# Performance work log

Measured on AMD Instinct MI355X. Metric: run time of the kernel, lower is better.

Reference implementation:

```python
import jax, jax.numpy as jnp
import numpy as np

# graph constants
B, V, CG, K, H, IN = 4, 6250, 25000, 3, 64, 2
NUM_LIT = B * 2 * V          # 50_000 literal nodes
NUM_CLS = B * CG             # 100_000 clause nodes
E = K * NUM_CLS              # 300_000 (l2c, c2l) edge pairs
NUM_ROUND = 3
DEMON = float(np.sqrt(H))    # self.demon = sqrt(hidden_size)


def setup_inputs() -> dict:
    key = jax.random.key(0)
    ks = jax.random.split(key, 12)
    rng = np.random.default_rng(0)
    # each clause has K literal endpoints; edges stay inside their own graph
    cls_idx = np.repeat(np.arange(NUM_CLS), K)
    g = cls_idx // CG
    lit_idx = g * 2 * V + rng.integers(0, 2 * V, size=E)

    def lin(k, fi, fo):
        return (jax.random.normal(k, (fi, fo), jnp.float32) / np.sqrt(fi)).astype(jnp.float32)

    return {
        "feat_l2c": jax.random.normal(ks[0], (E, IN), jnp.float32),
        "feat_c2l": jax.random.normal(ks[1], (E, IN), jnp.float32),
        "lit_idx": jnp.asarray(lit_idx, jnp.int32),
        "cls_idx": jnp.asarray(cls_idx, jnp.int32),
        "W_l2c_init": lin(ks[2], IN, H), "b_l2c_init": jnp.zeros((H,), jnp.float32),
        "W_c2l_init": lin(ks[3], IN, H), "b_c2l_init": jnp.zeros((H,), jnp.float32),
        "msgl_W": (jax.random.normal(ks[4], (3, H, H), jnp.float32) / np.sqrt(H)).astype(jnp.float32),
        "msgl_b": jnp.zeros((3, H), jnp.float32),
        "merge_W0": lin(ks[5], 2 * H, H), "merge_b0": jnp.zeros((H,), jnp.float32),
        "merge_Wr": (jax.random.normal(ks[6], (2, H, H), jnp.float32) / np.sqrt(H)).astype(jnp.float32),
        "merge_br": jnp.zeros((2, H), jnp.float32),
        "msgc_W": (jax.random.normal(ks[7], (3, H, H), jnp.float32) / np.sqrt(H)).astype(jnp.float32),
        "msgc_b": jnp.zeros((3, H), jnp.float32),
        "ro_W": (jax.random.normal(ks[8], (2, H, H), jnp.float32) / np.sqrt(H)).astype(jnp.float32),
        "ro_b": jnp.zeros((2, H), jnp.float32),
        "ro_W2": lin(ks[9], H, 1), "ro_b2": jnp.zeros((1,), jnp.float32),
    }


def _mlp3(x, W, b):  # 3-layer MLP, ReLU between layers (num_fc = 3)
    x = jax.nn.relu(x @ W[0] + b[0])
    x = jax.nn.relu(x @ W[1] + b[1])
    return x @ W[2] + b[2]


def reference(feat_l2c, feat_c2l, lit_idx, cls_idx,
              W_l2c_init, b_l2c_init, W_c2l_init, b_c2l_init,
              msgl_W, msgl_b, merge_W0, merge_b0, merge_Wr, merge_br,
              msgc_W, msgc_b, ro_W, ro_b, ro_W2, ro_b2):
    # init edge embeddings (l2c_init / c2l_init linear layers)
    h_l2c = feat_l2c @ W_l2c_init + b_l2c_init   # [E, H]
    h_c2l = feat_c2l @ W_c2l_init + b_c2l_init   # [E, H]

    for _ in range(NUM_ROUND):
        # literal update: aggregate incoming c2l messages, exclude self edge (BP-style)
        agg_l = jax.ops.segment_sum(h_c2l, lit_idx, num_segments=NUM_LIT)   # [NUM_LIT, H]
        m = _mlp3((agg_l[lit_idx] - h_c2l) / DEMON, msgl_W, msgl_b)          # [E, H]
        x = jax.nn.relu(jnp.concatenate([m, h_l2c], axis=-1) @ merge_W0 + merge_b0)
        x = jax.nn.relu(x @ merge_Wr[0] + merge_br[0])
        h_l2c = x @ merge_Wr[1] + merge_br[1]                                # l2c_merge_update
        # clause update
        agg_c = jax.ops.segment_sum(h_l2c, cls_idx, num_segments=NUM_CLS)   # [NUM_CLS, H]
        h_c2l = _mlp3((agg_c[cls_idx] - h_l2c) / DEMON, msgc_W, msgc_b)

    # u_add_e_sum with zero node feats == scatter-add edge emb to dst;
    # literal nodes only receive c2l edges
    l_emb = jax.ops.segment_sum(h_c2l, lit_idx, num_segments=NUM_LIT)        # [NUM_LIT, H]
    # segment_reduce(num_variable*2, ..., 'mean') over per-graph literal blocks (uniform sizes)
    l_mean = l_emb.reshape(B, 2 * V, H).mean(axis=1)                          # [B, H]
    x = jax.nn.relu(l_mean @ ro_W[0] + ro_b[0])
    x = jax.nn.relu(x @ ro_W[1] + ro_b[1])
    return jax.nn.sigmoid(x @ ro_W2 + ro_b2).squeeze(-1)                      # [B]
```

## Files before the change

### kernel.cpp

```cpp
#include <hip/hip_runtime.h>
#include <hip/hip_bf16.h>
#include <stdint.h>

#define EDGES   300000
#define NLIT    50000
#define NGRAPH  4
#define EPG     75000
#define HDIM    64

#define OFF_HL2C   0
#define OFF_HC2L   38400000
#define OFF_AGG    76800000
#define OFF_WT     89600000
#define OFF_ROACC  89681920
#define OFF_CNT    89682944
#define OFF_CSROFF 89882944
#define OFF_CURSOR 90082948
#define OFF_EIDX   90282948
#define OFF_BSUM   91482948
#define OFF_BBASE  91484000

#define WT_TOTAL    40960
#define WT_CLS_ELEM 28672

#define LIT_WBYTES (7 * 8192)
#define CLS_WBYTES (3 * 8192)
#define EPB3       512
#define GRID_EDGE  ((EDGES + EPB3 - 1) / EPB3)

#define SCAN_BLOCKS ((NLIT + 255) / 256)

typedef __attribute__((ext_vector_type(8)))  short          s16x8;
typedef __attribute__((ext_vector_type(8)))  unsigned short u16x8;
typedef __attribute__((ext_vector_type(4)))  unsigned short u16x4;
typedef __attribute__((ext_vector_type(4)))  float          f32x4;
typedef __attribute__((ext_vector_type(16))) float          f32x16;

__device__ __forceinline__ f32x16 mfma32(s16x8 a, s16x8 b, f32x16 c) {
    return __builtin_amdgcn_mfma_f32_32x32x16_bf16(a, b, c, 0, 0, 0);
}
__device__ __forceinline__ float bf2f(unsigned short s) {
    union { unsigned int u; float f; } v; v.u = ((unsigned int)s) << 16; return v.f;
}
__device__ __forceinline__ unsigned short f2bf(float f) {
    union { __hip_bfloat16 b; unsigned short s; } v;
    v.b = __float2bfloat16(f);
    return v.s;
}
__device__ __forceinline__ unsigned pk2(float a, float b) {
    return (unsigned)f2bf(a) | ((unsigned)f2bf(b) << 16);
}

__device__ __forceinline__ void layer32(const char* __restrict__ unitBase,
                                        const float* __restrict__ biasL,
                                        const s16x8 (&bin)[4], f32x16 (&acc)[2],
                                        int eL, int hi)
{
#pragma unroll
    for (int t = 0; t < 2; ++t)
#pragma unroll
        for (int g = 0; g < 4; ++g) {
            f32x4 bv = *(const f32x4*)(biasL + 32 * t + 8 * g + 4 * hi);
#pragma unroll
            for (int r = 0; r < 4; ++r) acc[t][4 * g + r] = bv[r];
        }
#pragma unroll
    for (int kb = 0; kb < 4; ++kb)
#pragma unroll
        for (int t = 0; t < 2; ++t) {
            int row = 32 * t + eL;
            s16x8 a = *(const s16x8*)(unitBase + row * 128 +
                                      ((32 * kb + 16 * hi) ^ ((row & 7) << 4)));
            acc[t] = mfma32(a, bin[kb], acc[t]);
        }
}

template<bool RELU>
__device__ __forceinline__ void relayout32(f32x16 (&acc)[2], s16x8 (&bout)[4],
                                           int bpidx, int hi)
{
    if (RELU) {
#pragma unroll
        for (int t = 0; t < 2; ++t)
#pragma unroll
            for (int i = 0; i < 16; ++i) acc[t][i] = fmaxf(acc[t][i], 0.f);
    }
#pragma unroll
    for (int kb = 0; kb < 4; ++kb) {
        int m0 = 2 * kb, m1 = 2 * kb + 1;
        int t0 = m0 >> 2, g0 = m0 & 3, t1 = m1 >> 2, g1 = m1 & 3;
        unsigned A0 = pk2(acc[t0][4 * g0 + 0], acc[t0][4 * g0 + 1]);
        unsigned A1 = pk2(acc[t0][4 * g0 + 2], acc[t0][4 * g0 + 3]);
        unsigned B0 = pk2(acc[t1][4 * g1 + 0], acc[t1][4 * g1 + 1]);
        unsigned B1 = pk2(acc[t1][4 * g1 + 2], acc[t1][4 * g1 + 3]);
        unsigned pA0 = (unsigned)__builtin_amdgcn_ds_bpermute(bpidx, (int)A0);
        unsigned pA1 = (unsigned)__builtin_amdgcn_ds_bpermute(bpidx, (int)A1);
        unsigned pB0 = (unsigned)__builtin_amdgcn_ds_bpermute(bpidx, (int)B0);
        unsigned pB1 = (unsigned)__builtin_amdgcn_ds_bpermute(bpidx, (int)B1);
        union { unsigned w[4]; s16x8 v; } u;
        u.w[0] = hi ? pB0 : A0;
        u.w[1] = hi ? pB1 : A1;
        u.w[2] = hi ? B0 : pA0;
        u.w[3] = hi ? B1 : pA1;
        bout[kb] = u.v;
    }
}

__device__ __forceinline__ void store32(const f32x16 (&acc)[2],
                                        unsigned short* __restrict__ dst, int hi)
{
#pragma unroll
    for (int t = 0; t < 2; ++t)
#pragma unroll
        for (int g = 0; g < 4; ++g) {
            u16x4 p;
#pragma unroll
            for (int r = 0; r < 4; ++r) p[r] = f2bf(acc[t][4 * g + r]);
            *(u16x4*)(dst + 32 * t + 8 * g + 4 * hi) = p;
        }
}

__global__ __launch_bounds__(256) void prep_weights(
    const float* __restrict__ msgl_W, const float* __restrict__ merge_W0,
    const float* __restrict__ merge_Wr, const float* __restrict__ msgc_W,
    unsigned short* __restrict__ wT)
{
    int gid = blockIdx.x * 256 + threadIdx.x;
    if (gid >= WT_TOTAL) return;
    int unit = gid >> 12;
    int o = (gid >> 6) & 63;
    int csw = gid & 63;
    int i = csw ^ ((o & 7) << 3);
    float v;
    if (unit < 3)       v = msgl_W[unit * 4096 + i * 64 + o];
    else if (unit < 5)  v = merge_W0[((unit - 3) * 64 + i) * 64 + o];
    else if (unit < 7)  v = merge_Wr[(unit - 5) * 4096 + i * 64 + o];
    else                v = msgc_W[(unit - 7) * 4096 + i * 64 + o];
    wT[gid] = f2bf(v);
}

__global__ __launch_bounds__(256) void csr_hist(const int* __restrict__ lit_idx,
                                                int* __restrict__ cnt)
{
    int e = blockIdx.x * 256 + threadIdx.x;
    if (e < EDGES) atomicAdd(&cnt[lit_idx[e]], 1);
}

__global__ __launch_bounds__(256) void scan1(const int* __restrict__ cnt,
                                             int* __restrict__ bsum)
{
    __shared__ int red[4];
    int i = blockIdx.x * 256 + threadIdx.x;
    int s = (i < NLIT) ? cnt[i] : 0;
#pragma unroll
    for (int off = 1; off < 64; off <<= 1) s += __shfl_xor(s, off, 64);
    if ((threadIdx.x & 63) == 0) red[threadIdx.x >> 6] = s;
    __syncthreads();
    if (threadIdx.x == 0) bsum[blockIdx.x] = red[0] + red[1] + red[2] + red[3];
}

__global__ __launch_bounds__(256) void scan2(const int* __restrict__ bsum,
                                             int* __restrict__ bbase)
{
    __shared__ int tmp[256];
    int t = threadIdx.x;
    int v = (t < SCAN_BLOCKS) ? bsum[t] : 0;
    tmp[t] = v;
    __syncthreads();
#pragma unroll
    for (int off = 1; off < 256; off <<= 1) {
        int add = (t >= off) ? tmp[t - off] : 0;
        __syncthreads();
        tmp[t] += add;
        __syncthreads();
    }
    if (t < SCAN_BLOCKS) bbase[t] = tmp[t] - v;
}

__global__ __launch_bounds__(256) void scan3(const int* __restrict__ cnt,
                                             const int* __restrict__ bbase,
                                             int* __restrict__ off,
                                             int* __restrict__ cursor)
{
    __shared__ int tmp[256];
    int t = threadIdx.x;
    int i = blockIdx.x * 256 + t;
    int v = (i < NLIT) ? cnt[i] : 0;
    tmp[t] = v;
    __syncthreads();
#pragma unroll
    for (int offs = 1; offs < 256; offs <<= 1) {
        int add = (t >= offs) ? tmp[t - offs] : 0;
        __syncthreads();
        tmp[t] += add;
        __syncthreads();
    }
    if (i < NLIT) {
        int ex = bbase[blockIdx.x] + tmp[t] - v;
        off[i] = ex; cursor[i] = ex;
    }
    if (i == NLIT - 1) off[NLIT] = EDGES;
}

__global__ __launch_bounds__(256) void csr_scatter(const int* __restrict__ lit_idx,
                                                   int* __restrict__ cursor,
                                                   int* __restrict__ eidx)
{
    int e = blockIdx.x * 256 + threadIdx.x;
    if (e >= EDGES) return;
    int pos = atomicAdd(&cursor[lit_idx[e]], 1);
    eidx[pos] = e;
}

__global__ __launch_bounds__(256) void aggregate(const unsigned short* __restrict__ h_c2l,
                                                 const int* __restrict__ off,
                                                 const int* __restrict__ eidx,
                                                 float* __restrict__ agg)
{
    int t = threadIdx.x;
    int lane8 = t & 7;
    int lit = blockIdx.x * 32 + (t >> 3);
    if (lit >= NLIT) return;
    int lo = off[lit], hi = off[lit + 1];
    float s[8] = {0, 0, 0, 0, 0, 0, 0, 0};
    int i = lo;
    for (; i + 4 <= hi; i += 4) {
        int e0 = eidx[i], e1 = eidx[i + 1], e2 = eidx[i + 2], e3 = eidx[i + 3];
        u16x8 v0 = *(const u16x8*)(h_c2l + e0 * 64 + lane8 * 8);
        u16x8 v1 = *(const u16x8*)(h_c2l + e1 * 64 + lane8 * 8);
        u16x8 v2 = *(const u16x8*)(h_c2l + e2 * 64 + lane8 * 8);
        u16x8 v3 = *(const u16x8*)(h_c2l + e3 * 64 + lane8 * 8);
#pragma unroll
        for (int j = 0; j < 8; ++j)
            s[j] += (bf2f(v0[j]) + bf2f(v1[j])) + (bf2f(v2[j]) + bf2f(v3[j]));
    }
    for (; i < hi; ++i) {
        int e = eidx[i];
        u16x8 hv = *(const u16x8*)(h_c2l + e * 64 + lane8 * 8);
#pragma unroll
        for (int j = 0; j < 8; ++j) s[j] += bf2f(hv[j]);
    }
    f32x4 a0, a1;
    a0[0] = s[0]; a0[1] = s[1]; a0[2] = s[2]; a0[3] = s[3];
    a1[0] = s[4]; a1[1] = s[5]; a1[2] = s[6]; a1[3] = s[7];
    *(f32x4*)(agg + lit * 64 + lane8 * 8)     = a0;
    *(f32x4*)(agg + lit * 64 + lane8 * 8 + 4) = a1;
}

__global__ __launch_bounds__(256) void init_kernel(
    const float* __restrict__ feat_l2c, const float* __restrict__ feat_c2l,
    const float* __restrict__ W_l2c, const float* __restrict__ b_l2c,
    const float* __restrict__ W_c2l, const float* __restrict__ b_c2l,
    unsigned short* __restrict__ h_l2c, unsigned short* __restrict__ h_c2l)
{
    int gid = blockIdx.x * 256 + threadIdx.x;
    if (gid >= EDGES * 8) return;
    int e = gid >> 3, fo = (gid & 7) << 3;
    float2 fl = *(const float2*)(feat_l2c + e * 2);
    float2 fc = *(const float2*)(feat_c2l + e * 2);

    u16x8 outl, outc;
#pragma unroll
    for (int j = 0; j < 8; ++j) {
        float wl0 = W_l2c[fo + j], wl1 = W_l2c[64 + fo + j];
        float wc0 = W_c2l[fo + j], wc1 = W_c2l[64 + fo + j];
        float vl = fl.x * wl0 + fl.y * wl1 + b_l2c[fo + j];
        float vc = fc.x * wc0 + fc.y * wc1 + b_c2l[fo + j];
        outl[j] = f2bf(vl);
        outc[j] = f2bf(vc);
    }
    *(u16x8*)(h_l2c + e * 64 + fo) = outl;
    *(u16x8*)(h_c2l + e * 64 + fo) = outc;
}

__global__ __launch_bounds__(1024, 4) void lit_update(
    const unsigned short* __restrict__ h_c2l,
    unsigned short* __restrict__ h_l2c,
    const float* __restrict__ agg,
    const int* __restrict__ lit_idx,
    const unsigned short* __restrict__ wT,
    const float* __restrict__ msgl_b,
    const float* __restrict__ merge_b0,
    const float* __restrict__ merge_br)
{
    __shared__ __align__(16) char lds[LIT_WBYTES + 384 * 4];
    int tid = threadIdx.x;
    for (int c = tid; c < LIT_WBYTES / 16; c += 1024)
        *(u16x8*)(lds + c * 16) = *(const u16x8*)(wT + c * 8);
    float* ldsBias = (float*)(lds + LIT_WBYTES);
    if (tid < 384) {
        float v;
        if (tid < 192)      v = msgl_b[tid];
        else if (tid < 256) v = merge_b0[tid - 192];
        else                v = merge_br[tid - 256];
        ldsBias[tid] = v;
    }
    __syncthreads();

    int wv = tid >> 6, lane = tid & 63;
    int eL = lane & 31, hi = lane >> 5;
    int bpidx = (lane ^ 32) << 2;
    int base = blockIdx.x * EPB3 + wv * 32;
    if (base >= EDGES) return;
    int e = base + eL;
    int lit = lit_idx[e];

    s16x8 hfrag[4];
#pragma unroll
    for (int k = 0; k < 4; ++k)
        hfrag[k] = *(const s16x8*)(h_l2c + e * 64 + 16 * k + 8 * hi);

    s16x8 binp[4];
#pragma unroll
    for (int k = 0; k < 4; ++k) {
        int f0 = 16 * k + 8 * hi;
        f32x4 a0 = *(const f32x4*)(agg + lit * 64 + f0);
        f32x4 a1 = *(const f32x4*)(agg + lit * 64 + f0 + 4);
        u16x8 hv = *(const u16x8*)(h_c2l + e * 64 + f0);
        s16x8 b;
#pragma unroll
        for (int j = 0; j < 4; ++j) b[j]     = (short)f2bf((a0[j] - bf2f(hv[j]))     * 0.125f);
#pragma unroll
        for (int j = 0; j < 4; ++j) b[4 + j] = (short)f2bf((a1[j] - bf2f(hv[4 + j])) * 0.125f);
        binp[k] = b;
    }

    f32x16 acc[2];
    s16x8 bf[4];
    layer32(lds,            ldsBias,       binp, acc, eL, hi);
    relayout32<true >(acc, bf, bpidx, hi);
    layer32(lds + 8192,     ldsBias + 64,  bf, acc, eL, hi);
    relayout32<true >(acc, bf, bpidx, hi);
    layer32(lds + 2 * 8192, ldsBias + 128, bf, acc, eL, hi);
    relayout32<false>(acc, bf, bpidx, hi);

#pragma unroll
    for (int t = 0; t < 2; ++t)
#pragma unroll
        for (int g = 0; g < 4; ++g) {
            f32x4 bv = *(const f32x4*)(ldsBias + 192 + 32 * t + 8 * g + 4 * hi);
#pragma unroll
            for (int r = 0; r < 4; ++r) acc[t][4 * g + r] = bv[r];
        }
#pragma unroll
    for (int kb = 0; kb < 8; ++kb) {
        const char* ub = lds + (3 + (kb >> 2)) * 8192;
        s16x8 bop = (kb < 4) ? bf[kb] : hfrag[kb - 4];
#pragma unroll
        for (int t = 0; t < 2; ++t) {
            int row = 32 * t + eL;
            s16x8 a = *(const s16x8*)(ub + row * 128 +
                                      ((32 * (kb & 3) + 16 * hi) ^ ((row & 7) << 4)));
            acc[t] = mfma32(a, bop, acc[t]);
        }
    }
    relayout32<true>(acc, bf, bpidx, hi);
    layer32(lds + 5 * 8192, ldsBias + 256, bf, acc, eL, hi);
    relayout32<true>(acc, bf, bpidx, hi);
    layer32(lds + 6 * 8192, ldsBias + 320, bf, acc, eL, hi);

    store32(acc, h_l2c + e * 64, hi);
}

__global__ __launch_bounds__(1024, 4) void clause_update(
    const unsigned short* __restrict__ h_l2c,
    unsigned short* __restrict__ h_c2l,
    const unsigned short* __restrict__ msgcT,
    const float* __restrict__ msgc_b)
{
    __shared__ __align__(16) char lds[CLS_WBYTES + 192 * 4];
    int tid = threadIdx.x;
    for (int c = tid; c < CLS_WBYTES / 16; c += 1024)
        *(u16x8*)(lds + c * 16) = *(const u16x8*)(msgcT + c * 8);
    float* ldsBias = (float*)(lds + CLS_WBYTES);
    if (tid < 192) ldsBias[tid] = msgc_b[tid];
    __syncthreads();

    int wv = tid >> 6, lane = tid & 63;
    int eL = lane & 31, hi = lane >> 5;
    int bpidx = (lane ^ 32) << 2;
    int base = blockIdx.x * EPB3 + wv * 32;
    if (base >= EDGES) return;
    int e = base + eL;

    int c3 = (e / 3) * 3;
    int d = e - c3;
    int e1 = c3 + (d == 0 ? 1 : 0);
    int e2 = c3 + (d == 2 ? 1 : 2);

    s16x8 binp[4];
#pragma unroll
    for (int k = 0; k < 4; ++k) {
        int f0 = 16 * k + 8 * hi;
        u16x8 h1 = *(const u16x8*)(h_l2c + e1 * 64 + f0);
        u16x8 h2 = *(const u16x8*)(h_l2c + e2 * 64 + f0);
        s16x8 b;
#pragma unroll
        for (int j = 0; j < 8; ++j)
            b[j] = (short)f2bf((bf2f(h1[j]) + bf2f(h2[j])) * 0.125f);
        binp[k] = b;
    }

    f32x16 acc[2];
    s16x8 bf[4];
    layer32(lds,            ldsBias,       binp, acc, eL, hi);
    relayout32<true>(acc, bf, bpidx, hi);
    layer32(lds + 8192,     ldsBias + 64,  bf, acc, eL, hi);
    relayout32<true>(acc, bf, bpidx, hi);
    layer32(lds + 2 * 8192, ldsBias + 128, bf, acc, eL, hi);

    store32(acc, h_c2l + e * 64, hi);
}

__global__ __launch_bounds__(256) void readout_sum(
    const unsigned short* __restrict__ h_c2l, float* __restrict__ ro_acc)
{
    __shared__ float lsum[32][64];
    int g = blockIdx.x >> 6, chunk = blockIdx.x & 63;
    int t = threadIdx.x;
    int fg = t & 7, el = t >> 3;
    float s[8] = {0, 0, 0, 0, 0, 0, 0, 0};
    for (int idx = chunk * 32 + el; idx < EPG; idx += 2048) {
        u16x8 hv = *(const u16x8*)(h_c2l + (g * EPG + idx) * 64 + fg * 8);
#pragma unroll
        for (int j = 0; j < 8; ++j) s[j] += bf2f(hv[j]);
    }
#pragma unroll
    for (int j = 0; j < 8; ++j) lsum[el][fg * 8 + j] = s[j];
    __syncthreads();
    if (t < 64) {
        float tot = 0.f;
#pragma unroll 8
        for (int r = 0; r < 32; ++r) tot += lsum[r][t];
        atomicAdd(&ro_acc[g * 64 + t], tot);
    }
}

__global__ __launch_bounds__(256) void readout_mlp(
    const float* __restrict__ ro_acc, const float* __restrict__ ro_W,
    const float* __restrict__ ro_b, const float* __restrict__ ro_W2,
    const float* __restrict__ ro_b2, float* __restrict__ out)
{
    __shared__ float xb[NGRAPH][HDIM];
    __shared__ float yb[NGRAPH][HDIM];
    int g = threadIdx.x >> 6;
    int j = threadIdx.x & 63;
    xb[g][j] = ro_acc[g * HDIM + j] * (1.0f / 12500.0f);
    __syncthreads();
    float a = ro_b[j];
#pragma unroll 8
    for (int k = 0; k < HDIM; ++k) a += xb[g][k] * ro_W[k * HDIM + j];
    a = fmaxf(a, 0.0f);
    yb[g][j] = a;
    __syncthreads();
    float a2 = ro_b[HDIM + j];
#pragma unroll 8
    for (int k = 0; k < HDIM; ++k) a2 += yb[g][k] * ro_W[4096 + k * HDIM + j];
    a2 = fmaxf(a2, 0.0f);
    float p = a2 * ro_W2[j];
#pragma unroll
    for (int off = 32; off > 0; off >>= 1) p += __shfl_down(p, off, 64);
    if (j == 0) out[g] = 1.0f / (1.0f + expf(-(p + ro_b2[0])));
}

extern "C" void kernel_launch(void* const* d_in, const int* in_sizes, int n_in,
                              void* d_out, int out_size, void* d_ws, size_t ws_size,
                              hipStream_t stream)
{
    const float* feat_l2c = (const float*)d_in[0];
    const float* feat_c2l = (const float*)d_in[1];
    const int*   lit_idx  = (const int*)d_in[2];
    const float* W_l2c    = (const float*)d_in[4];
    const float* b_l2c    = (const float*)d_in[5];
    const float* W_c2l    = (const float*)d_in[6];
    const float* b_c2l    = (const float*)d_in[7];
    const float* msgl_W   = (const float*)d_in[8];
    const float* msgl_b   = (const float*)d_in[9];
    const float* merge_W0 = (const float*)d_in[10];
    const float* merge_b0 = (const float*)d_in[11];
    const float* merge_Wr = (const float*)d_in[12];
    const float* merge_br = (const float*)d_in[13];
    const float* msgc_W   = (const float*)d_in[14];
    const float* msgc_b   = (const float*)d_in[15];
    const float* ro_W     = (const float*)d_in[16];
    const float* ro_b     = (const float*)d_in[17];
    const float* ro_W2    = (const float*)d_in[18];
    const float* ro_b2    = (const float*)d_in[19];

    char* ws = (char*)d_ws;
    unsigned short* h_l2c  = (unsigned short*)(ws + OFF_HL2C);
    unsigned short* h_c2l  = (unsigned short*)(ws + OFF_HC2L);
    float*          agg    = (float*)(ws + OFF_AGG);
    unsigned short* wT     = (unsigned short*)(ws + OFF_WT);
    float*          ro_acc = (float*)(ws + OFF_ROACC);
    int*            cnt    = (int*)(ws + OFF_CNT);
    int*            csroff = (int*)(ws + OFF_CSROFF);
    int*            cursor = (int*)(ws + OFF_CURSOR);
    int*            eidx   = (int*)(ws + OFF_EIDX);
    int*            bsum   = (int*)(ws + OFF_BSUM);
    int*            bbase  = (int*)(ws + OFF_BBASE);

    hipMemsetAsync(cnt, 0, NLIT * sizeof(int), stream);
    hipMemsetAsync(ro_acc, 0, NGRAPH * 64 * sizeof(float), stream);

    prep_weights<<<(WT_TOTAL + 255) / 256, 256, 0, stream>>>(msgl_W, merge_W0, merge_Wr, msgc_W, wT);

    csr_hist<<<(EDGES + 255) / 256, 256, 0, stream>>>(lit_idx, cnt);
    scan1<<<SCAN_BLOCKS, 256, 0, stream>>>(cnt, bsum);
    scan2<<<1, 256, 0, stream>>>(bsum, bbase);
    scan3<<<SCAN_BLOCKS, 256, 0, stream>>>(cnt, bbase, csroff, cursor);
    csr_scatter<<<(EDGES + 255) / 256, 256, 0, stream>>>(lit_idx, cursor, eidx);

    init_kernel<<<EDGES * 8 / 256, 256, 0, stream>>>(feat_l2c, feat_c2l, W_l2c, b_l2c,
                                                     W_c2l, b_c2l, h_l2c, h_c2l);
    for (int r = 0; r < 3; ++r) {
        aggregate<<<(NLIT + 31) / 32, 256, 0, stream>>>(h_c2l, csroff, eidx, agg);
        lit_update<<<GRID_EDGE, 1024, 0, stream>>>(h_c2l, h_l2c, agg, lit_idx, wT,
                                                   msgl_b, merge_b0, merge_br);
        clause_update<<<GRID_EDGE, 1024, 0, stream>>>(h_l2c, h_c2l, wT + WT_CLS_ELEM, msgc_b);
    }
    readout_sum<<<256, 256, 0, stream>>>(h_c2l, ro_acc);
    readout_mlp<<<1, 256, 0, stream>>>(ro_acc, ro_W, ro_b, ro_W2, ro_b2, (float*)d_out);
}
```

Baseline: 352.9 us.

## Store aggregates in bf16, halve block size, and trim bpermutes in relayout

Four changes ship together. The per-literal aggregate buffer is now written and read as bf16 instead of fp32, which halves its write and gather traffic at some cost in precision of the summed messages. The edge-update kernels drop from 1024 to 512 threads per block (256 edges per block), and their LDS weight preload loop is unrolled. The accumulator relayout now selects the value to send before the ds_bpermute, so each k-block needs two bpermutes instead of four. Smaller blocks reload the shared weights more often, and with LDS-limited residency they may lower the number of resident waves.

```diff
diff --git a/kernel.cpp b/kernel.cpp
--- a/kernel.cpp
+++ b/kernel.cpp
@@ -25,8 +25,8 @@
 
 #define LIT_WBYTES (7 * 8192)
 #define CLS_WBYTES (3 * 8192)
-#define EPB3       512
-#define GRID_EDGE  ((EDGES + EPB3 - 1) / EPB3)
+#define EPB2       256
+#define GRID_EDGE  ((EDGES + EPB2 - 1) / EPB2)
 
 #define SCAN_BLOCKS ((NLIT + 255) / 256)
 
@@ -49,30 +49,6 @@
 }
 __device__ __forceinline__ unsigned pk2(float a, float b) {
     return (unsigned)f2bf(a) | ((unsigned)f2bf(b) << 16);
-}
-
-__device__ __forceinline__ void layer32(const char* __restrict__ unitBase,
-                                        const float* __restrict__ biasL,
-                                        const s16x8 (&bin)[4], f32x16 (&acc)[2],
-                                        int eL, int hi)
-{
-#pragma unroll
-    for (int t = 0; t < 2; ++t)
-#pragma unroll
-        for (int g = 0; g < 4; ++g) {
-            f32x4 bv = *(const f32x4*)(biasL + 32 * t + 8 * g + 4 * hi);
-#pragma unroll
-            for (int r = 0; r < 4; ++r) acc[t][4 * g + r] = bv[r];
-        }
-#pragma unroll
-    for (int kb = 0; kb < 4; ++kb)
-#pragma unroll
-        for (int t = 0; t < 2; ++t) {
-            int row = 32 * t + eL;
-            s16x8 a = *(const s16x8*)(unitBase + row * 128 +
-                                      ((32 * kb + 16 * hi) ^ ((row & 7) << 4)));
-            acc[t] = mfma32(a, bin[kb], acc[t]);
-        }
 }
 
 template<bool RELU>
@@ -93,15 +69,15 @@
         unsigned A1 = pk2(acc[t0][4 * g0 + 2], acc[t0][4 * g0 + 3]);
         unsigned B0 = pk2(acc[t1][4 * g1 + 0], acc[t1][4 * g1 + 1]);
         unsigned B1 = pk2(acc[t1][4 * g1 + 2], acc[t1][4 * g1 + 3]);
-        unsigned pA0 = (unsigned)__builtin_amdgcn_ds_bpermute(bpidx, (int)A0);
-        unsigned pA1 = (unsigned)__builtin_amdgcn_ds_bpermute(bpidx, (int)A1);
-        unsigned pB0 = (unsigned)__builtin_amdgcn_ds_bpermute(bpidx, (int)B0);
-        unsigned pB1 = (unsigned)__builtin_amdgcn_ds_bpermute(bpidx, (int)B1);
+        unsigned s0 = hi ? A0 : B0;
+        unsigned s1 = hi ? A1 : B1;
+        unsigned p0 = (unsigned)__builtin_amdgcn_ds_bpermute(bpidx, (int)s0);
+        unsigned p1 = (unsigned)__builtin_amdgcn_ds_bpermute(bpidx, (int)s1);
         union { unsigned w[4]; s16x8 v; } u;
-        u.w[0] = hi ? pB0 : A0;
-        u.w[1] = hi ? pB1 : A1;
-        u.w[2] = hi ? B0 : pA0;
-        u.w[3] = hi ? B1 : pA1;
+        u.w[0] = hi ? p0 : A0;
+        u.w[1] = hi ? p1 : A1;
+        u.w[2] = hi ? B0 : p0;
+        u.w[3] = hi ? B1 : p1;
         bout[kb] = u.v;
     }
 }
@@ -117,6 +93,30 @@
 #pragma unroll
             for (int r = 0; r < 4; ++r) p[r] = f2bf(acc[t][4 * g + r]);
             *(u16x4*)(dst + 32 * t + 8 * g + 4 * hi) = p;
+        }
+}
+
+__device__ __forceinline__ void layer32(const char* __restrict__ unitBase,
+                                        const float* __restrict__ biasL,
+                                        const s16x8 (&bin)[4], f32x16 (&acc)[2],
+                                        int eL, int hi)
+{
+#pragma unroll
+    for (int t = 0; t < 2; ++t)
+#pragma unroll
+        for (int g = 0; g < 4; ++g) {
+            f32x4 bv = *(const f32x4*)(biasL + 32 * t + 8 * g + 4 * hi);
+#pragma unroll
+            for (int r = 0; r < 4; ++r) acc[t][4 * g + r] = bv[r];
+        }
+#pragma unroll
+    for (int kb = 0; kb < 4; ++kb)
+#pragma unroll
+        for (int t = 0; t < 2; ++t) {
+            int row = 32 * t + eL;
+            s16x8 a = *(const s16x8*)(unitBase + row * 128 +
+                                      ((32 * kb + 16 * hi) ^ ((row & 7) << 4)));
+            acc[t] = mfma32(a, bin[kb], acc[t]);
         }
 }
 
@@ -215,7 +215,7 @@
 __global__ __launch_bounds__(256) void aggregate(const unsigned short* __restrict__ h_c2l,
                                                  const int* __restrict__ off,
                                                  const int* __restrict__ eidx,
-                                                 float* __restrict__ agg)
+                                                 unsigned short* __restrict__ agg)
 {
     int t = threadIdx.x;
     int lane8 = t & 7;
@@ -240,11 +240,10 @@
 #pragma unroll
         for (int j = 0; j < 8; ++j) s[j] += bf2f(hv[j]);
     }
-    f32x4 a0, a1;
-    a0[0] = s[0]; a0[1] = s[1]; a0[2] = s[2]; a0[3] = s[3];
-    a1[0] = s[4]; a1[1] = s[5]; a1[2] = s[6]; a1[3] = s[7];
-    *(f32x4*)(agg + lit * 64 + lane8 * 8)     = a0;
-    *(f32x4*)(agg + lit * 64 + lane8 * 8 + 4) = a1;
+    u16x8 o;
+#pragma unroll
+    for (int j = 0; j < 8; ++j) o[j] = f2bf(s[j]);
+    *(u16x8*)(agg + lit * 64 + lane8 * 8) = o;
 }
 
 __global__ __launch_bounds__(256) void init_kernel(
@@ -273,10 +272,10 @@
     *(u16x8*)(h_c2l + e * 64 + fo) = outc;
 }
 
-__global__ __launch_bounds__(1024, 4) void lit_update(
+__global__ __launch_bounds__(512, 4) void lit_update(
     const unsigned short* __restrict__ h_c2l,
     unsigned short* __restrict__ h_l2c,
-    const float* __restrict__ agg,
+    const unsigned short* __restrict__ agg,
     const int* __restrict__ lit_idx,
     const unsigned short* __restrict__ wT,
     const float* __restrict__ msgl_b,
@@ -285,8 +284,11 @@
 {
     __shared__ __align__(16) char lds[LIT_WBYTES + 384 * 4];
     int tid = threadIdx.x;
-    for (int c = tid; c < LIT_WBYTES / 16; c += 1024)
-        *(u16x8*)(lds + c * 16) = *(const u16x8*)(wT + c * 8);
+#pragma unroll
+    for (int c = 0; c < 7; ++c) {
+        int idx = c * 512 + tid;
+        *(u16x8*)(lds + idx * 16) = *(const u16x8*)(wT + idx * 8);
+    }
     float* ldsBias = (float*)(lds + LIT_WBYTES);
     if (tid < 384) {
         float v;
@@ -300,7 +302,7 @@
     int wv = tid >> 6, lane = tid & 63;
     int eL = lane & 31, hi = lane >> 5;
     int bpidx = (lane ^ 32) << 2;
-    int base = blockIdx.x * EPB3 + wv * 32;
+    int base = blockIdx.x * EPB2 + wv * 32;
     if (base >= EDGES) return;
     int e = base + eL;
     int lit = lit_idx[e];
@@ -314,14 +316,12 @@
 #pragma unroll
     for (int k = 0; k < 4; ++k) {
         int f0 = 16 * k + 8 * hi;
-        f32x4 a0 = *(const f32x4*)(agg + lit * 64 + f0);
-        f32x4 a1 = *(const f32x4*)(agg + lit * 64 + f0 + 4);
+        u16x8 ag = *(const u16x8*)(agg + lit * 64 + f0);
         u16x8 hv = *(const u16x8*)(h_c2l + e * 64 + f0);
         s16x8 b;
 #pragma unroll
-        for (int j = 0; j < 4; ++j) b[j]     = (short)f2bf((a0[j] - bf2f(hv[j]))     * 0.125f);
-#pragma unroll
-        for (int j = 0; j < 4; ++j) b[4 + j] = (short)f2bf((a1[j] - bf2f(hv[4 + j])) * 0.125f);
+        for (int j = 0; j < 8; ++j)
+            b[j] = (short)f2bf((bf2f(ag[j]) - bf2f(hv[j])) * 0.125f);
         binp[k] = b;
     }
 
@@ -362,7 +362,7 @@
     store32(acc, h_l2c + e * 64, hi);
 }
 
-__global__ __launch_bounds__(1024, 4) void clause_update(
+__global__ __launch_bounds__(512, 4) void clause_update(
     const unsigned short* __restrict__ h_l2c,
     unsigned short* __restrict__ h_c2l,
     const unsigned short* __restrict__ msgcT,
@@ -370,8 +370,11 @@
 {
     __shared__ __align__(16) char lds[CLS_WBYTES + 192 * 4];
     int tid = threadIdx.x;
-    for (int c = tid; c < CLS_WBYTES / 16; c += 1024)
-        *(u16x8*)(lds + c * 16) = *(const u16x8*)(msgcT + c * 8);
+#pragma unroll
+    for (int c = 0; c < 3; ++c) {
+        int idx = c * 512 + tid;
+        *(u16x8*)(lds + idx * 16) = *(const u16x8*)(msgcT + idx * 8);
+    }
     float* ldsBias = (float*)(lds + CLS_WBYTES);
     if (tid < 192) ldsBias[tid] = msgc_b[tid];
     __syncthreads();
@@ -379,7 +382,7 @@
     int wv = tid >> 6, lane = tid & 63;
     int eL = lane & 31, hi = lane >> 5;
     int bpidx = (lane ^ 32) << 2;
-    int base = blockIdx.x * EPB3 + wv * 32;
+    int base = blockIdx.x * EPB2 + wv * 32;
     if (base >= EDGES) return;
     int e = base + eL;
 
@@ -490,7 +493,7 @@
     char* ws = (char*)d_ws;
     unsigned short* h_l2c  = (unsigned short*)(ws + OFF_HL2C);
     unsigned short* h_c2l  = (unsigned short*)(ws + OFF_HC2L);
-    float*          agg    = (float*)(ws + OFF_AGG);
+    unsigned short* agg    = (unsigned short*)(ws + OFF_AGG);
     unsigned short* wT     = (unsigned short*)(ws + OFF_WT);
     float*          ro_acc = (float*)(ws + OFF_ROACC);
     int*            cnt    = (int*)(ws + OFF_CNT);
@@ -515,9 +518,9 @@
                                                      W_c2l, b_c2l, h_l2c, h_c2l);
     for (int r = 0; r < 3; ++r) {
         aggregate<<<(NLIT + 31) / 32, 256, 0, stream>>>(h_c2l, csroff, eidx, agg);
-        lit_update<<<GRID_EDGE, 1024, 0, stream>>>(h_c2l, h_l2c, agg, lit_idx, wT,
-                                                   msgl_b, merge_b0, merge_br);
-        clause_update<<<GRID_EDGE, 1024, 0, stream>>>(h_l2c, h_c2l, wT + WT_CLS_ELEM, msgc_b);
+        lit_update<<<GRID_EDGE, 512, 0, stream>>>(h_c2l, h_l2c, agg, lit_idx, wT,
+                                                  msgl_b, merge_b0, merge_br);
+        clause_update<<<GRID_EDGE, 512, 0, stream>>>(h_l2c, h_c2l, wT + WT_CLS_ELEM, msgc_b);
     }
     readout_sum<<<256, 256, 0, stream>>>(h_c2l, ro_acc);
     readout_mlp<<<1, 256, 0, stream>>>(ro_acc, ro_W, ro_b, ro_W2, ro_b2, (float*)d_out);
```

Result: faster. 311.6 us (median of 2 runs) (-11.7%).
